# Kernel tuning notes

Measured on AMD Instinct MI355X. Metric: run time of the kernel, lower is better.

The kernel has to match this reference:

```python
import jax, jax.numpy as jnp
import numpy as np

EPS = 1e-5


def setup_inputs() -> dict:
    key = jax.random.key(0)
    S, B, I, H, D = 256, 512, 64, 128, 32
    ks = jax.random.split(key, 12)

    def w(k, shape, fan):
        return jax.random.normal(k, shape, jnp.float32) * (fan ** -0.5)

    lengths = jax.random.randint(ks[0], (B,), 1, S + 1)
    lengths = lengths.at[0].set(S)  # ensure max length == S
    return {
        'x': jax.random.normal(ks[1], (S, B, I), jnp.float32),
        'x_d': jax.random.normal(ks[2], (S, B, D), jnp.float32),
        'lengths': lengths,
        'bn_g': jnp.ones((I,), jnp.float32), 'bn_b': jnp.zeros((I,), jnp.float32),
        'bnd_g': jnp.ones((D,), jnp.float32), 'bnd_b': jnp.zeros((D,), jnp.float32),
        'Wih': w(ks[3], (3 * H, I), I), 'Whh': w(ks[4], (3 * H, H), H),
        'bih': jnp.zeros((3 * H,), jnp.float32), 'bhh': jnp.zeros((3 * H,), jnp.float32),
        'attn_W': w(ks[5], (H, H), H), 'attn_b': jnp.zeros((H,), jnp.float32),
        'W1': w(ks[6], (H, H + D), H + D), 'b1': jnp.zeros((H,), jnp.float32),
        'W2': w(ks[7], (H, H), H), 'b2': jnp.zeros((H,), jnp.float32),
        'W3': w(ks[8], (H, H), H), 'b3': jnp.zeros((H,), jnp.float32),
    }


def reference(x, x_d, lengths, bn_g, bn_b, bnd_g, bnd_b, Wih, Whh, bih, bhh,
              attn_W, attn_b, W1, b1, W2, b2, W3, b3):
    S, B, I = x.shape
    H = Whh.shape[1]
    mask = jnp.arange(S)[:, None] < lengths[None, :]          # [S,B] valid-token mask
    mf = mask[..., None].astype(x.dtype)                       # [S,B,1]
    cnt = mf.sum()

    def bn(v, g, b):  # training-mode BatchNorm1d over the packed (valid) tokens
        mu = (v * mf).sum((0, 1)) / cnt
        var = (((v - mu) * mf) ** 2).sum((0, 1)) / cnt
        return (v - mu) * jax.lax.rsqrt(var + EPS) * g + b

    xn = bn(x, bn_g, bn_b)
    xdn = bn(x_d, bnd_g, bnd_b)

    # --- GRU (PyTorch gate order r,z,n) over padded sequence with mask ---
    h0 = jnp.zeros((B, H), x.dtype)

    def step(h, inp):
        xt, mt = inp                                           # xt [B,I], mt [B,1]
        gi = xt @ Wih.T + bih
        gh = h @ Whh.T + bhh
        ir, iz, inn = jnp.split(gi, 3, axis=-1)
        hr, hz, hn = jnp.split(gh, 3, axis=-1)
        r = jax.nn.sigmoid(ir + hr)
        z = jax.nn.sigmoid(iz + hz)
        n = jnp.tanh(inn + r * hn)
        hnew = (1 - z) * n + z * h
        hnext = jnp.where(mt, hnew, h)                         # carry last valid state
        return hnext, jnp.where(mt, hnew, 0.0)                 # padded outputs are 0

    h_last, ys = jax.lax.scan(step, h0, (xn, mf))              # ys [S,B,H]

    # --- Dynamic_Attention: per step i only position j=i survives the causal
    # mask in column k=i, so the dim-0 softmax is over one element -> weight 1.
    # Keep fc in the graph (zero grad, same as torch) via a size-1 softmax. ---
    s = (ys @ attn_W.T + attn_b).sum(-1)                       # [S,B]
    attn = jax.nn.softmax(s[..., None, None], axis=-2)[..., 0, :]  # ones [S,B,1]
    y = attn * ys

    # --- per-token MLP (dropout = identity at eval), vectorized over all tokens ---
    z0 = jnp.concatenate([y, xdn], axis=-1)                    # [S,B,H+D]
    d = jax.nn.relu(z0 @ W1.T + b1)
    d = jax.nn.relu(d @ W2.T + b2)
    d = jax.nn.relu(d @ W3.T + b3)
    out = d * mf                                               # zero padded positions
    return out, h_last[None]                                   # hidden: [1,B,H]
```

## Files before the change

### kernel.cpp

```cpp
#include <hip/hip_runtime.h>
#include <hip/hip_bf16.h>

#define SS 256
#define BB 512
#define II 64
#define HH 128
#define DD 32

typedef __attribute__((ext_vector_type(8))) short short8;
typedef __attribute__((ext_vector_type(4))) float f32x4;

__device__ __forceinline__ short f2bf(float f) {
    unsigned u = __builtin_bit_cast(unsigned, f);
    u += 0x7FFFu + ((u >> 16) & 1u);
    return (short)(u >> 16);
}
__device__ __forceinline__ int pack2bf(float a, float b) {
    return (int)((((unsigned)(unsigned short)f2bf(b)) << 16) |
                  ((unsigned)(unsigned short)f2bf(a)));
}
__device__ __forceinline__ short8 load8bf(const float* p) {
    short8 r;
#pragma unroll
    for (int j = 0; j < 8; ++j) r[j] = f2bf(p[j]);
    return r;
}

__device__ __forceinline__ void sync_lds() {
    __builtin_amdgcn_s_waitcnt(0xc07f);
    __builtin_amdgcn_s_barrier();
}

#define SWZ(colv, off) ((off) ^ (((colv) & 7) << 3))

__global__ __launch_bounds__(256) void stats_kernel(
    const float* __restrict__ x, const float* __restrict__ xd,
    const int* __restrict__ lengths,
    float* __restrict__ px, float* __restrict__ pd,
    unsigned* __restrict__ counter,
    const float* __restrict__ bn_g, const float* __restrict__ bn_b,
    const float* __restrict__ bnd_g, const float* __restrict__ bnd_b,
    float* __restrict__ der)
{
    __shared__ int s_len[BB];
    __shared__ f32x4 red_s[256];
    __shared__ f32x4 red_q[256];
    __shared__ unsigned s_last;

    const int tid = threadIdx.x;
    const int blk = blockIdx.x;
    for (int i = tid; i < BB; i += 256) s_len[i] = lengths[i];
    __syncthreads();

    f32x4 s = {0.f, 0.f, 0.f, 0.f};
    f32x4 q = {0.f, 0.f, 0.f, 0.f};

    if (blk < 256) {
        const int c4   = tid & 15;
        const int rowg = tid >> 4;
        const float* base = x + (size_t)blk * BB * II + c4 * 4;
#pragma unroll 8
        for (int it = 0; it < 32; ++it) {
            const int b = it * 16 + rowg;
            const f32x4 xv = *(const f32x4*)&base[(size_t)b * II];
            const f32x4 xm = (blk < s_len[b]) ? xv : (f32x4){0.f, 0.f, 0.f, 0.f};
            s += xm;
            q += xm * xm;
        }
        red_s[tid] = s; red_q[tid] = q;
        __syncthreads();
#pragma unroll
        for (int g = 8; g >= 1; g >>= 1) {
            if (rowg < g) {
                red_s[tid] += red_s[tid + 16 * g];
                red_q[tid] += red_q[tid + 16 * g];
            }
            __syncthreads();
        }
        if (rowg == 0) {
            const f32x4 fs = red_s[tid], fq = red_q[tid];
            float* row = px + (size_t)blk * 128;
#pragma unroll
            for (int j = 0; j < 4; ++j) {
                __hip_atomic_store(&row[c4 * 4 + j],      fs[j], __ATOMIC_RELAXED, __HIP_MEMORY_SCOPE_AGENT);
                __hip_atomic_store(&row[64 + c4 * 4 + j], fq[j], __ATOMIC_RELAXED, __HIP_MEMORY_SCOPE_AGENT);
            }
        }
    } else {
        const int bx   = blk - 256;
        const int c4   = tid & 7;
        const int rowg = tid >> 3;
        const int r0   = bx * 1024;
        const float* base = xd + (size_t)r0 * DD + c4 * 4;
#pragma unroll 8
        for (int it = 0; it < 32; ++it) {
            const int rr  = it * 32 + rowg;
            const int row = r0 + rr;
            const int b   = row & (BB - 1);
            const int si  = row >> 9;
            const f32x4 xv = *(const f32x4*)&base[(size_t)rr * DD];
            const f32x4 xm = (si < s_len[b]) ? xv : (f32x4){0.f, 0.f, 0.f, 0.f};
            s += xm;
            q += xm * xm;
        }
        red_s[tid] = s; red_q[tid] = q;
        __syncthreads();
#pragma unroll
        for (int g = 16; g >= 1; g >>= 1) {
            if (rowg < g) {
                red_s[tid] += red_s[tid + 8 * g];
                red_q[tid] += red_q[tid + 8 * g];
            }
            __syncthreads();
        }
        if (rowg == 0) {
            const f32x4 fs = red_s[tid], fq = red_q[tid];
            float* row = pd + (size_t)bx * 64;
#pragma unroll
            for (int j = 0; j < 4; ++j) {
                __hip_atomic_store(&row[c4 * 4 + j],      fs[j], __ATOMIC_RELAXED, __HIP_MEMORY_SCOPE_AGENT);
                __hip_atomic_store(&row[32 + c4 * 4 + j], fq[j], __ATOMIC_RELAXED, __HIP_MEMORY_SCOPE_AGENT);
            }
        }
    }

    __threadfence();
    __syncthreads();
    if (tid == 0) {
        unsigned old = atomicAdd(counter, 1u);
        s_last = (old == 383u) ? 1u : 0u;
    }
    __syncthreads();
    if (!s_last) return;
    __threadfence();

    __shared__ double s_sum[192];
    if (tid < 128) {
        const float* col = px + tid;
        double a = 0.0;
#pragma unroll 8
        for (int r = 0; r < 256; ++r)
            a += (double)__hip_atomic_load(&col[(size_t)r * 128], __ATOMIC_RELAXED, __HIP_MEMORY_SCOPE_AGENT);
        s_sum[tid] = a;
    } else if (tid < 192) {
        const float* col = pd + (tid - 128);
        double a = 0.0;
#pragma unroll 8
        for (int r = 0; r < 128; ++r)
            a += (double)__hip_atomic_load(&col[(size_t)r * 64], __ATOMIC_RELAXED, __HIP_MEMORY_SCOPE_AGENT);
        s_sum[tid] = a;
    }
    __shared__ int redc[256];
    int cs = 0;
    for (int i = tid; i < BB; i += 256) cs += s_len[i];
    redc[tid] = cs;
    __syncthreads();
    for (int off = 128; off; off >>= 1) {
        if (tid < off) redc[tid] += redc[tid + off];
        __syncthreads();
    }
    const double inv = 1.0 / (double)redc[0];
    if (tid < 64) {
        const double mu  = s_sum[tid] * inv;
        const double var = s_sum[64 + tid] * inv - mu * mu;
        const float  rs  = rsqrtf((float)(var + 1e-5));
        const float  a   = rs * bn_g[tid];
        der[tid]      = a;
        der[64 + tid] = bn_b[tid] - (float)mu * a;
    } else if (tid < 96) {
        const int i = tid - 64;
        const double mu  = s_sum[128 + i] * inv;
        const double var = s_sum[160 + i] * inv - mu * mu;
        const float  rs  = rsqrtf((float)(var + 1e-5));
        const float  a   = rs * bnd_g[i];
        der[128 + i] = a;
        der[160 + i] = bnd_b[i] - (float)mu * a;
    }
}

__global__ __launch_bounds__(512, 2) void gru_kernel(
    const float* __restrict__ x, const int* __restrict__ lengths,
    const float* __restrict__ Wih, const float* __restrict__ Whh,
    const float* __restrict__ bih, const float* __restrict__ bhh,
    const float* __restrict__ der,
    float* __restrict__ ys, float* __restrict__ hlast)
{
    __shared__ __align__(16) short hbf[2][16 * 128];
    __shared__ __align__(16) short xbf[2][16 * 64];

    const int tid  = threadIdx.x;
    const int w    = tid >> 6;
    const int l    = tid & 63;
    const int col  = l & 15;
    const int quad = l >> 4;
    const int b0   = blockIdx.x * 16;
    const int ur   = 16 * w + col;
    const int g0   = 16 * w + quad * 4;

    short8 WR[6], WZ[6], WNh[4], WNx[2];
#pragma unroll
    for (int ks = 0; ks < 4; ++ks) {
        const int ko = ks * 32 + quad * 8;
        WR[ks]  = load8bf(&Whh[(size_t)ur * HH + ko]);
        WZ[ks]  = load8bf(&Whh[(size_t)(HH + ur) * HH + ko]);
        WNh[ks] = load8bf(&Whh[(size_t)(2 * HH + ur) * HH + ko]);
    }
#pragma unroll
    for (int ks = 0; ks < 2; ++ks) {
        const int ko = ks * 32 + quad * 8;
        WR[4 + ks] = load8bf(&Wih[(size_t)ur * II + ko]);
        WZ[4 + ks] = load8bf(&Wih[(size_t)(HH + ur) * II + ko]);
        WNx[ks]    = load8bf(&Wih[(size_t)(2 * HH + ur) * II + ko]);
    }
    float br_[4], bz_[4], bnh_[4], bnx_[4];
#pragma unroll
    for (int r = 0; r < 4; ++r) {
        const int g = g0 + r;
        br_[r]  = bih[g] + bhh[g];
        bz_[r]  = bih[HH + g] + bhh[HH + g];
        bnh_[r] = bhh[2 * HH + g];
        bnx_[r] = bih[2 * HH + g];
    }
    const int len = lengths[b0 + col];

    const int srow = tid >> 5, scol = (tid & 31) * 2;
    const float ax0 = der[scol],      ax1 = der[scol + 1];
    const float cx0 = der[64 + scol], cx1 = der[64 + scol + 1];

    for (int i = tid; i < 16 * 128 / 2; i += 512) ((int*)hbf[0])[i] = 0;
    float hreg[4] = {0.f, 0.f, 0.f, 0.f};
    {
        const float2 xv = *(const float2*)&x[(size_t)(b0 + srow) * II + scol];
        *(int*)&xbf[0][SWZ(srow, srow * 64 + scol)] =
            pack2bf(fmaf(xv.x, ax0, cx0), fmaf(xv.y, ax1, cx1));
    }
    sync_lds();

    int p = 0;
    for (int t = 0; t < SS; ++t) {
        float2 xv;
        if (t + 1 < SS)
            xv = *(const float2*)&x[(size_t)((t + 1) * BB + b0 + srow) * II + scol];

        short8 Hf[4];
#pragma unroll
        for (int ks = 0; ks < 4; ++ks)
            Hf[ks] = *(const short8*)&hbf[p][SWZ(col, col * 128 + ks * 32 + quad * 8)];
        const short8 XN0 = *(const short8*)&xbf[p][SWZ(col, col * 64 + quad * 8)];
        const short8 XN1 = *(const short8*)&xbf[p][SWZ(col, col * 64 + 32 + quad * 8)];

        f32x4 ar  = {br_[0],  br_[1],  br_[2],  br_[3]};
        f32x4 az  = {bz_[0],  bz_[1],  bz_[2],  bz_[3]};
        f32x4 anh = {bnh_[0], bnh_[1], bnh_[2], bnh_[3]};
        f32x4 anx = {bnx_[0], bnx_[1], bnx_[2], bnx_[3]};
#pragma unroll
        for (int ks = 0; ks < 4; ++ks) {
            ar  = __builtin_amdgcn_mfma_f32_16x16x32_bf16(WR[ks],  Hf[ks], ar,  0, 0, 0);
            az  = __builtin_amdgcn_mfma_f32_16x16x32_bf16(WZ[ks],  Hf[ks], az,  0, 0, 0);
            anh = __builtin_amdgcn_mfma_f32_16x16x32_bf16(WNh[ks], Hf[ks], anh, 0, 0, 0);
        }
        ar  = __builtin_amdgcn_mfma_f32_16x16x32_bf16(WR[4],  XN0, ar,  0, 0, 0);
        ar  = __builtin_amdgcn_mfma_f32_16x16x32_bf16(WR[5],  XN1, ar,  0, 0, 0);
        az  = __builtin_amdgcn_mfma_f32_16x16x32_bf16(WZ[4],  XN0, az,  0, 0, 0);
        az  = __builtin_amdgcn_mfma_f32_16x16x32_bf16(WZ[5],  XN1, az,  0, 0, 0);
        anx = __builtin_amdgcn_mfma_f32_16x16x32_bf16(WNx[0], XN0, anx, 0, 0, 0);
        anx = __builtin_amdgcn_mfma_f32_16x16x32_bf16(WNx[1], XN1, anx, 0, 0, 0);

        const bool valid = (t < len);
#pragma unroll
        for (int r = 0; r < 4; ++r) {
            const float rg = __builtin_amdgcn_rcpf(1.f + __expf(-ar[r]));
            const float zg = __builtin_amdgcn_rcpf(1.f + __expf(-az[r]));
            const float nv = anx[r] + rg * anh[r];
            const float ng = 1.f - 2.f * __builtin_amdgcn_rcpf(1.f + __expf(2.f * nv));
            const float hnew = (1.f - zg) * ng + zg * hreg[r];
            hreg[r] = valid ? hnew : hreg[r];
        }
        {
            float4 o;
            o.x = hreg[0]; o.y = hreg[1]; o.z = hreg[2]; o.w = hreg[3];
            *(float4*)&ys[((size_t)t * BB + b0 + col) * HH + g0] = o;
            int2 pk;
            pk.x = pack2bf(hreg[0], hreg[1]);
            pk.y = pack2bf(hreg[2], hreg[3]);
            *(int2*)&hbf[p ^ 1][SWZ(col, col * 128 + g0)] = pk;
        }
        if (t + 1 < SS)
            *(int*)&xbf[p ^ 1][SWZ(srow, srow * 64 + scol)] =
                pack2bf(fmaf(xv.x, ax0, cx0), fmaf(xv.y, ax1, cx1));

        sync_lds();
        p ^= 1;
    }

    {
        float4 hl;
        hl.x = hreg[0]; hl.y = hreg[1]; hl.z = hreg[2]; hl.w = hreg[3];
        *(float4*)&hlast[(size_t)(b0 + col) * HH + g0] = hl;
    }
}

__global__ __launch_bounds__(512, 2) void mlp_kernel(
    const float* __restrict__ xd, const int* __restrict__ lengths,
    const float* __restrict__ W1, const float* __restrict__ b1v,
    const float* __restrict__ W2, const float* __restrict__ b2v,
    const float* __restrict__ W3, const float* __restrict__ b3v,
    const float* __restrict__ der, float* io)
{
    __shared__ __align__(16) short z0[2][16 * 168];
    __shared__ __align__(16) short d1b[2][16 * 128];
    __shared__ __align__(16) short d2b[2][16 * 128];

    const int tid  = threadIdx.x;
    const int w    = tid >> 6;
    const int l    = tid & 63;
    const int col  = l & 15;
    const int quad = l >> 4;
    const int ur   = 16 * w + col;
    const int g0   = 16 * w + quad * 4;

    short8 F1[5], F2[4], F3[4];
#pragma unroll
    for (int ks = 0; ks < 5; ++ks)
        F1[ks] = load8bf(&W1[(size_t)ur * 160 + ks * 32 + quad * 8]);
#pragma unroll
    for (int ks = 0; ks < 4; ++ks) {
        const int ko = ks * 32 + quad * 8;
        F2[ks] = load8bf(&W2[(size_t)ur * HH + ko]);
        F3[ks] = load8bf(&W3[(size_t)ur * HH + ko]);
    }
    float bb1_[4], bb2_[4], bb3_[4];
#pragma unroll
    for (int r = 0; r < 4; ++r) {
        bb1_[r] = b1v[g0 + r]; bb2_[r] = b2v[g0 + r]; bb3_[r] = b3v[g0 + r];
    }

    const int yrow = tid >> 5, yc = (tid & 31) * 4;
    const int drow = tid >> 4, dcol = (tid & 15) * 2;
    float ad0 = 0.f, ad1 = 0.f, cd0 = 0.f, cd1 = 0.f;
    if (tid < 256) {
        ad0 = der[128 + dcol]; ad1 = der[128 + dcol + 1];
        cd0 = der[160 + dcol]; cd1 = der[160 + dcol + 1];
    }

    const int tile0 = blockIdx.x * 16;

    {
        const size_t tok0 = (size_t)tile0 * 16;
        const float4 yv = *(const float4*)&io[(tok0 + yrow) * HH + yc];
        int2 pk;
        pk.x = pack2bf(yv.x, yv.y);
        pk.y = pack2bf(yv.z, yv.w);
        *(int2*)&z0[0][yrow * 168 + yc] = pk;
        if (tid < 256) {
            const float2 dv = *(const float2*)&xd[(tok0 + drow) * DD + dcol];
            *(int*)&z0[0][drow * 168 + HH + dcol] =
                pack2bf(fmaf(dv.x, ad0, cd0), fmaf(dv.y, ad1, cd1));
        }
    }
    sync_lds();

    int p = 0;
    for (int it = 0; it <= 17; ++it) {
        float4 yv; float2 dv;
        const int nt = it + 1;
        if (nt <= 15) {
            const size_t tok0n = (size_t)(tile0 + nt) * 16;
            yv = *(const float4*)&io[(tok0n + yrow) * HH + yc];
            if (tid < 256) dv = *(const float2*)&xd[(tok0n + drow) * DD + dcol];
        }

        f32x4 a1 = {bb1_[0], bb1_[1], bb1_[2], bb1_[3]};
#pragma unroll
        for (int ks = 0; ks < 5; ++ks)
            a1 = __builtin_amdgcn_mfma_f32_16x16x32_bf16(
                F1[ks], *(const short8*)&z0[p][col * 168 + ks * 32 + quad * 8], a1, 0, 0, 0);
        {
            int2 pk;
            pk.x = pack2bf(fmaxf(a1[0], 0.f), fmaxf(a1[1], 0.f));
            pk.y = pack2bf(fmaxf(a1[2], 0.f), fmaxf(a1[3], 0.f));
            *(int2*)&d1b[p ^ 1][SWZ(col, col * 128 + g0)] = pk;
        }

        f32x4 a2 = {bb2_[0], bb2_[1], bb2_[2], bb2_[3]};
#pragma unroll
        for (int ks = 0; ks < 4; ++ks)
            a2 = __builtin_amdgcn_mfma_f32_16x16x32_bf16(
                F2[ks], *(const short8*)&d1b[p][SWZ(col, col * 128 + ks * 32 + quad * 8)], a2, 0, 0, 0);
        {
            int2 pk;
            pk.x = pack2bf(fmaxf(a2[0], 0.f), fmaxf(a2[1], 0.f));
            pk.y = pack2bf(fmaxf(a2[2], 0.f), fmaxf(a2[3], 0.f));
            *(int2*)&d2b[p ^ 1][SWZ(col, col * 128 + g0)] = pk;
        }

        f32x4 a3 = {bb3_[0], bb3_[1], bb3_[2], bb3_[3]};
#pragma unroll
        for (int ks = 0; ks < 4; ++ks)
            a3 = __builtin_amdgcn_mfma_f32_16x16x32_bf16(
                F3[ks], *(const short8*)&d2b[p][SWZ(col, col * 128 + ks * 32 + quad * 8)], a3, 0, 0, 0);
        if (it >= 2) {
            const int tok0 = (tile0 + it - 2) * 16;
            const int tI = tok0 >> 9;
            const int bI = tok0 & (BB - 1);
            const bool v = tI < lengths[bI + col];
            float4 o;
            o.x = v ? fmaxf(a3[0], 0.f) : 0.f;
            o.y = v ? fmaxf(a3[1], 0.f) : 0.f;
            o.z = v ? fmaxf(a3[2], 0.f) : 0.f;
            o.w = v ? fmaxf(a3[3], 0.f) : 0.f;
            *(float4*)&io[((size_t)tok0 + col) * HH + g0] = o;
        }

        if (nt <= 15) {
            int2 pk;
            pk.x = pack2bf(yv.x, yv.y);
            pk.y = pack2bf(yv.z, yv.w);
            *(int2*)&z0[p ^ 1][yrow * 168 + yc] = pk;
            if (tid < 256)
                *(int*)&z0[p ^ 1][drow * 168 + HH + dcol] =
                    pack2bf(fmaf(dv.x, ad0, cd0), fmaf(dv.y, ad1, cd1));
        }
        sync_lds();
        p ^= 1;
    }
}

extern "C" void kernel_launch(void* const* d_in, const int* in_sizes, int n_in,
                              void* d_out, int out_size, void* d_ws, size_t ws_size,
                              hipStream_t stream)
{
    (void)in_sizes; (void)n_in; (void)out_size;
    const float* x     = (const float*)d_in[0];
    const float* xd    = (const float*)d_in[1];
    const int*   lens  = (const int*)d_in[2];
    const float* bn_g  = (const float*)d_in[3];
    const float* bn_b  = (const float*)d_in[4];
    const float* bnd_g = (const float*)d_in[5];
    const float* bnd_b = (const float*)d_in[6];
    const float* Wih   = (const float*)d_in[7];
    const float* Whh   = (const float*)d_in[8];
    const float* bih   = (const float*)d_in[9];
    const float* bhh   = (const float*)d_in[10];
    const float* W1    = (const float*)d_in[13];
    const float* b1    = (const float*)d_in[14];
    const float* W2    = (const float*)d_in[15];
    const float* b2    = (const float*)d_in[16];
    const float* W3    = (const float*)d_in[17];
    const float* b3    = (const float*)d_in[18];

    float* out   = (float*)d_out;
    float* hlast = out + (size_t)SS * BB * HH;

    unsigned* counter  = (unsigned*)((char*)d_ws + 1536);
    float*    der      = (float*)((char*)d_ws + 2048);
    float*    px       = (float*)((char*)d_ws + 4096);
    float*    pd       = px + 256 * 128;

    (void)hipMemsetAsync(d_ws, 0, 2048, stream);

    stats_kernel<<<384, 256, 0, stream>>>(x, xd, lens, px, pd, counter,
                                          bn_g, bn_b, bnd_g, bnd_b, der);

    gru_kernel<<<BB / 16, 512, 0, stream>>>(x, lens, Wih, Whh, bih, bhh, der,
                                            out, hlast);

    mlp_kernel<<<512, 512, 0, stream>>>(xd, lens, W1, b1, W2, b2, W3, b3,
                                        der, out);
}
```

Baseline: 446.1 us.

## Use hardware bf16 pack, padded LDS rows, and reorder GRU MFMAs

```diff
diff --git a/kernel.cpp b/kernel.cpp
--- a/kernel.cpp
+++ b/kernel.cpp
@@ -16,8 +16,9 @@
     return (short)(u >> 16);
 }
 __device__ __forceinline__ int pack2bf(float a, float b) {
-    return (int)((((unsigned)(unsigned short)f2bf(b)) << 16) |
-                  ((unsigned)(unsigned short)f2bf(a)));
+    int r;
+    asm("v_cvt_pk_bf16_f32 %0, %1, %2" : "=v"(r) : "v"(a), "v"(b));
+    return r;
 }
 __device__ __forceinline__ short8 load8bf(const float* p) {
     short8 r;
@@ -30,8 +31,6 @@
     __builtin_amdgcn_s_waitcnt(0xc07f);
     __builtin_amdgcn_s_barrier();
 }
-
-#define SWZ(colv, off) ((off) ^ (((colv) & 7) << 3))
 
 __global__ __launch_bounds__(256) void stats_kernel(
     const float* __restrict__ x, const float* __restrict__ xd,
@@ -185,8 +184,8 @@
     const float* __restrict__ der,
     float* __restrict__ ys, float* __restrict__ hlast)
 {
-    __shared__ __align__(16) short hbf[2][16 * 128];
-    __shared__ __align__(16) short xbf[2][16 * 64];
+    __shared__ __align__(16) short hbf[2][16 * 136];
+    __shared__ __align__(16) short xbf[2][16 * 72];
 
     const int tid  = threadIdx.x;
     const int w    = tid >> 6;
@@ -227,11 +226,11 @@
     const float ax0 = der[scol],      ax1 = der[scol + 1];
     const float cx0 = der[64 + scol], cx1 = der[64 + scol + 1];
 
-    for (int i = tid; i < 16 * 128 / 2; i += 512) ((int*)hbf[0])[i] = 0;
+    for (int i = tid; i < 16 * 136 / 2; i += 512) ((int*)hbf[0])[i] = 0;
     float hreg[4] = {0.f, 0.f, 0.f, 0.f};
     {
         const float2 xv = *(const float2*)&x[(size_t)(b0 + srow) * II + scol];
-        *(int*)&xbf[0][SWZ(srow, srow * 64 + scol)] =
+        *(int*)&xbf[0][srow * 72 + scol] =
             pack2bf(fmaf(xv.x, ax0, cx0), fmaf(xv.y, ax1, cx1));
     }
     sync_lds();
@@ -242,29 +241,30 @@
         if (t + 1 < SS)
             xv = *(const float2*)&x[(size_t)((t + 1) * BB + b0 + srow) * II + scol];
 
+        const short8 XN0 = *(const short8*)&xbf[p][col * 72 + quad * 8];
+        const short8 XN1 = *(const short8*)&xbf[p][col * 72 + 32 + quad * 8];
         short8 Hf[4];
 #pragma unroll
         for (int ks = 0; ks < 4; ++ks)
-            Hf[ks] = *(const short8*)&hbf[p][SWZ(col, col * 128 + ks * 32 + quad * 8)];
-        const short8 XN0 = *(const short8*)&xbf[p][SWZ(col, col * 64 + quad * 8)];
-        const short8 XN1 = *(const short8*)&xbf[p][SWZ(col, col * 64 + 32 + quad * 8)];
+            Hf[ks] = *(const short8*)&hbf[p][col * 136 + ks * 32 + quad * 8];
 
         f32x4 ar  = {br_[0],  br_[1],  br_[2],  br_[3]};
         f32x4 az  = {bz_[0],  bz_[1],  bz_[2],  bz_[3]};
         f32x4 anh = {bnh_[0], bnh_[1], bnh_[2], bnh_[3]};
         f32x4 anx = {bnx_[0], bnx_[1], bnx_[2], bnx_[3]};
-#pragma unroll
-        for (int ks = 0; ks < 4; ++ks) {
-            ar  = __builtin_amdgcn_mfma_f32_16x16x32_bf16(WR[ks],  Hf[ks], ar,  0, 0, 0);
-            az  = __builtin_amdgcn_mfma_f32_16x16x32_bf16(WZ[ks],  Hf[ks], az,  0, 0, 0);
-            anh = __builtin_amdgcn_mfma_f32_16x16x32_bf16(WNh[ks], Hf[ks], anh, 0, 0, 0);
-        }
+
         ar  = __builtin_amdgcn_mfma_f32_16x16x32_bf16(WR[4],  XN0, ar,  0, 0, 0);
         ar  = __builtin_amdgcn_mfma_f32_16x16x32_bf16(WR[5],  XN1, ar,  0, 0, 0);
         az  = __builtin_amdgcn_mfma_f32_16x16x32_bf16(WZ[4],  XN0, az,  0, 0, 0);
         az  = __builtin_amdgcn_mfma_f32_16x16x32_bf16(WZ[5],  XN1, az,  0, 0, 0);
         anx = __builtin_amdgcn_mfma_f32_16x16x32_bf16(WNx[0], XN0, anx, 0, 0, 0);
         anx = __builtin_amdgcn_mfma_f32_16x16x32_bf16(WNx[1], XN1, anx, 0, 0, 0);
+#pragma unroll
+        for (int ks = 0; ks < 4; ++ks) {
+            ar  = __builtin_amdgcn_mfma_f32_16x16x32_bf16(WR[ks],  Hf[ks], ar,  0, 0, 0);
+            az  = __builtin_amdgcn_mfma_f32_16x16x32_bf16(WZ[ks],  Hf[ks], az,  0, 0, 0);
+            anh = __builtin_amdgcn_mfma_f32_16x16x32_bf16(WNh[ks], Hf[ks], anh, 0, 0, 0);
+        }
 
         const bool valid = (t < len);
 #pragma unroll
@@ -273,7 +273,7 @@
             const float zg = __builtin_amdgcn_rcpf(1.f + __expf(-az[r]));
             const float nv = anx[r] + rg * anh[r];
             const float ng = 1.f - 2.f * __builtin_amdgcn_rcpf(1.f + __expf(2.f * nv));
-            const float hnew = (1.f - zg) * ng + zg * hreg[r];
+            const float hnew = ng + zg * (hreg[r] - ng);
             hreg[r] = valid ? hnew : hreg[r];
         }
         {
@@ -283,10 +283,10 @@
             int2 pk;
             pk.x = pack2bf(hreg[0], hreg[1]);
             pk.y = pack2bf(hreg[2], hreg[3]);
-            *(int2*)&hbf[p ^ 1][SWZ(col, col * 128 + g0)] = pk;
+            *(int2*)&hbf[p ^ 1][col * 136 + g0] = pk;
         }
         if (t + 1 < SS)
-            *(int*)&xbf[p ^ 1][SWZ(srow, srow * 64 + scol)] =
+            *(int*)&xbf[p ^ 1][srow * 72 + scol] =
                 pack2bf(fmaf(xv.x, ax0, cx0), fmaf(xv.y, ax1, cx1));
 
         sync_lds();
@@ -308,8 +308,8 @@
     const float* __restrict__ der, float* io)
 {
     __shared__ __align__(16) short z0[2][16 * 168];
-    __shared__ __align__(16) short d1b[2][16 * 128];
-    __shared__ __align__(16) short d2b[2][16 * 128];
+    __shared__ __align__(16) short d1b[2][16 * 136];
+    __shared__ __align__(16) short d2b[2][16 * 136];
 
     const int tid  = threadIdx.x;
     const int w    = tid >> 6;
@@ -379,26 +379,26 @@
             int2 pk;
             pk.x = pack2bf(fmaxf(a1[0], 0.f), fmaxf(a1[1], 0.f));
             pk.y = pack2bf(fmaxf(a1[2], 0.f), fmaxf(a1[3], 0.f));
-            *(int2*)&d1b[p ^ 1][SWZ(col, col * 128 + g0)] = pk;
+            *(int2*)&d1b[p ^ 1][col * 136 + g0] = pk;
         }
 
         f32x4 a2 = {bb2_[0], bb2_[1], bb2_[2], bb2_[3]};
 #pragma unroll
         for (int ks = 0; ks < 4; ++ks)
             a2 = __builtin_amdgcn_mfma_f32_16x16x32_bf16(
-                F2[ks], *(const short8*)&d1b[p][SWZ(col, col * 128 + ks * 32 + quad * 8)], a2, 0, 0, 0);
+                F2[ks], *(const short8*)&d1b[p][col * 136 + ks * 32 + quad * 8], a2, 0, 0, 0);
         {
             int2 pk;
             pk.x = pack2bf(fmaxf(a2[0], 0.f), fmaxf(a2[1], 0.f));
             pk.y = pack2bf(fmaxf(a2[2], 0.f), fmaxf(a2[3], 0.f));
-            *(int2*)&d2b[p ^ 1][SWZ(col, col * 128 + g0)] = pk;
+            *(int2*)&d2b[p ^ 1][col * 136 + g0] = pk;
         }
 
         f32x4 a3 = {bb3_[0], bb3_[1], bb3_[2], bb3_[3]};
 #pragma unroll
         for (int ks = 0; ks < 4; ++ks)
             a3 = __builtin_amdgcn_mfma_f32_16x16x32_bf16(
-                F3[ks], *(const short8*)&d2b[p][SWZ(col, col * 128 + ks * 32 + quad * 8)], a3, 0, 0, 0);
+                F3[ks], *(const short8*)&d2b[p][col * 136 + ks * 32 + quad * 8], a3, 0, 0, 0);
         if (it >= 2) {
             const int tok0 = (tile0 + it - 2) * 16;
             const int tI = tok0 >> 9;
@@ -430,7 +430,7 @@
                               void* d_out, int out_size, void* d_ws, size_t ws_size,
                               hipStream_t stream)
 {
-    (void)in_sizes; (void)n_in; (void)out_size;
+    (void)in_sizes; (void)n_in; (void)out_size; (void)ws_size;
     const float* x     = (const float*)d_in[0];
     const float* xd    = (const float*)d_in[1];
     const int*   lens  = (const int*)d_in[2];
```

Result: faster. 433.6 us (median of 2 runs) (-2.8%).
